# Kernel optimization log

Measured on AMD Instinct MI355X. Metric: run time of the kernel, lower is better.

The kernel has to match this reference:

```python
import jax, jax.numpy as jnp
import numpy as np

N_PTS = 65536   # input points
M = 4096        # sampled clusters (n_nodes)
K = 16          # knn neighbors
C_IN = 128
C_OUT = 256
BN_EPS = 1e-5


def setup_inputs() -> dict:
    key = jax.random.key(0)
    k1, k2, k3 = jax.random.split(key, 3)
    x = jax.random.normal(k1, (N_PTS, C_IN), jnp.float32)
    pos = jax.random.normal(k2, (N_PTS, 3), jnp.float32)
    batch = jnp.zeros((N_PTS,), jnp.int32)  # single point cloud
    W = jax.random.normal(k3, (C_IN, C_OUT), jnp.float32) / np.sqrt(C_IN)
    b = jnp.zeros((C_OUT,), jnp.float32)
    gamma = jnp.ones((C_OUT,), jnp.float32)
    beta = jnp.zeros((C_OUT,), jnp.float32)
    return {"x": x, "pos": pos, "batch": batch, "W": W, "b": b,
            "gamma": gamma, "beta": beta}


def _fps(pos, m):
    """Farthest point sampling starting from index 0. Returns m indices."""
    n = pos.shape[0]

    def step(carry, _):
        min_d, last = carry
        d = jnp.sum((pos - pos[last]) ** 2, axis=-1)  # [N]
        min_d = jnp.minimum(min_d, d)
        nxt = jnp.argmax(min_d).astype(jnp.int32)
        return (min_d, nxt), nxt

    init = (jnp.full((n,), jnp.inf, pos.dtype), jnp.int32(0))
    _, rest = jax.lax.scan(step, init, None, length=m - 1)
    return jnp.concatenate([jnp.zeros((1,), jnp.int32), rest])


def _knn(pos, sub_pos, k):
    """For each of M query points, indices of k nearest points in pos. [M, k]"""
    # squared euclidean distances, [M, N]
    d2 = (jnp.sum(sub_pos ** 2, -1, keepdims=True)
          - 2.0 * sub_pos @ pos.T
          + jnp.sum(pos ** 2, -1)[None, :])
    _, idx = jax.lax.top_k(-d2, k)
    return idx


def _mlp(x, W, b, gamma, beta):
    # Linear -> BatchNorm1d (training-mode batch stats, biased var) -> ReLU
    h = x @ W + b                      # [N, C_OUT]
    mu = jnp.mean(h, axis=0)
    var = jnp.mean((h - mu) ** 2, axis=0)
    h = gamma * (h - mu) * jax.lax.rsqrt(var + BN_EPS) + beta
    return jax.nn.relu(h)


def reference(x, pos, batch, W, b, gamma, beta):
    id_clusters = _fps(pos, M)                 # [M]
    sub_pos = pos[id_clusters]                 # [M, 3]
    sub_batch = batch[id_clusters]             # [M]
    nbr = _knn(pos, sub_pos, K)                # [M, K]
    h = _mlp(x, W, b, gamma, beta)             # [N, C_OUT]
    # gather + max-pool over each cluster's k neighbors (== scatter_max,
    # since knn emits exactly K neighbors per cluster, grouped by cluster)
    out = jnp.max(h[nbr], axis=1)              # [M, C_OUT]
    return out, sub_pos, sub_batch
```

## Files before the change

### kernel.cpp

```cpp
#include <hip/hip_runtime.h>
#include <hip/hip_bf16.h>

#define N_PTS 65536
#define MCLUS 4096
#define KNN   16
#define C_IN  128
#define C_OUT 256

typedef unsigned long long u64;
typedef unsigned u32;

#define WS_ID     0
#define WS_SLOTS  16384
#define WS_BBOX   49152
#define WS_CNT    49216
#define WS_OFS    51264
#define WS_NBR    53312
#define WS_PSUM   315456
#define WS_POS4   315456
#define WS_PSUMSQ 839744
#define WS_SCALE  1364032
#define WS_SHIFT  1365056

__device__ __forceinline__ u32 fkey(float v) {
    u32 u = __float_as_uint(v);
    return (u >> 31) ? ~u : (u | 0x80000000u);
}
__device__ __forceinline__ float funkey(u32 k) {
    u32 u = (k >> 31) ? (k & 0x7FFFFFFFu) : ~k;
    return __uint_as_float(u);
}

__global__ void init_kernel(int* __restrict__ id, u64* __restrict__ slots,
                            u32* __restrict__ bbox, int* __restrict__ cellcnt) {
    int t = threadIdx.x;
    for (int i = t; i < 4096; i += 1024) slots[i] = 0ull;
    if (t < 512) cellcnt[t] = 0;
    if (t < 3)   bbox[t] = 0xFFFFFFFFu;
    if (t >= 3 && t < 6) bbox[t] = 0u;
    if (t == 0) id[0] = 0;
}

__global__ __launch_bounds__(256) void bbox_kernel(const float* __restrict__ pos,
                                                   u32* __restrict__ bbox) {
    int t = blockIdx.x * 256 + threadIdx.x;
    u32 mn0 = 0xFFFFFFFFu, mn1 = 0xFFFFFFFFu, mn2 = 0xFFFFFFFFu;
    u32 mx0 = 0u, mx1 = 0u, mx2 = 0u;
    for (int i = t; i < N_PTS; i += 16384) {
        u32 k0 = fkey(pos[i*3+0]), k1 = fkey(pos[i*3+1]), k2 = fkey(pos[i*3+2]);
        mn0 = min(mn0, k0); mn1 = min(mn1, k1); mn2 = min(mn2, k2);
        mx0 = max(mx0, k0); mx1 = max(mx1, k1); mx2 = max(mx2, k2);
    }
    #pragma unroll
    for (int off = 32; off > 0; off >>= 1) {
        mn0 = min(mn0, (u32)__shfl_xor(mn0, off)); mx0 = max(mx0, (u32)__shfl_xor(mx0, off));
        mn1 = min(mn1, (u32)__shfl_xor(mn1, off)); mx1 = max(mx1, (u32)__shfl_xor(mx1, off));
        mn2 = min(mn2, (u32)__shfl_xor(mn2, off)); mx2 = max(mx2, (u32)__shfl_xor(mx2, off));
    }
    if ((threadIdx.x & 63) == 0) {
        atomicMin(&bbox[0], mn0); atomicMin(&bbox[1], mn1); atomicMin(&bbox[2], mn2);
        atomicMax(&bbox[3], mx0); atomicMax(&bbox[4], mx1); atomicMax(&bbox[5], mx2);
    }
}

__device__ __forceinline__ int cell_of(float x, float y, float z, const u32* bb) {
    float x0 = funkey(bb[0]), y0 = funkey(bb[1]), z0 = funkey(bb[2]);
    float x1 = funkey(bb[3]), y1 = funkey(bb[4]), z1 = funkey(bb[5]);
    float sx = 8.0f / fmaxf(x1 - x0, 1e-20f);
    float sy = 8.0f / fmaxf(y1 - y0, 1e-20f);
    float sz = 8.0f / fmaxf(z1 - z0, 1e-20f);
    int gx = min(max((int)((x - x0) * sx), 0), 7);
    int gy = min(max((int)((y - y0) * sy), 0), 7);
    int gz = min(max((int)((z - z0) * sz), 0), 7);
    int m = 0;
    #pragma unroll
    for (int k = 0; k < 3; ++k)
        m |= (((gx >> k) & 1) << (3*k + 2)) | (((gy >> k) & 1) << (3*k + 1)) | (((gz >> k) & 1) << (3*k));
    return m;
}

__global__ __launch_bounds__(256) void count_kernel(const float* __restrict__ pos,
                                                    const u32* __restrict__ bbox,
                                                    int* __restrict__ cellcnt) {
    int i = blockIdx.x * 256 + threadIdx.x;
    atomicAdd(&cellcnt[cell_of(pos[i*3+0], pos[i*3+1], pos[i*3+2], bbox)], 1);
}

__global__ __launch_bounds__(512) void scan_kernel(const int* __restrict__ cellcnt,
                                                   int* __restrict__ cellofs) {
    __shared__ int tmp[512];
    int t = threadIdx.x;
    int c = cellcnt[t];
    tmp[t] = c; __syncthreads();
    for (int off = 1; off < 512; off <<= 1) {
        int v = (t >= off) ? tmp[t - off] : 0;
        __syncthreads();
        tmp[t] += v;
        __syncthreads();
    }
    cellofs[t] = tmp[t] - c;
}

__global__ __launch_bounds__(256) void scatter_kernel(const float* __restrict__ pos,
                                                      const u32* __restrict__ bbox,
                                                      int* __restrict__ cellofs,
                                                      float4* __restrict__ pos4) {
    int i = blockIdx.x * 256 + threadIdx.x;
    float x = pos[i*3+0], y = pos[i*3+1], z = pos[i*3+2];
    int o = atomicAdd(&cellofs[cell_of(x, y, z, bbox)], 1);
    pos4[o] = make_float4(x, y, z, __int_as_float(i));
}

__device__ __forceinline__ float dist3(float ax, float ay, float az,
                                       float bx, float by, float bz) {
    float dx = __fsub_rn(ax, bx), dy = __fsub_rn(ay, by), dz = __fsub_rn(az, bz);
    return __fadd_rn(__fadd_rn(__fmul_rn(dx, dx), __fmul_rn(dy, dy)), __fmul_rn(dz, dz));
}

__device__ __forceinline__ u32 wave_max_u32(u32 v) {
    #pragma unroll
    for (int off = 32; off > 0; off >>= 1) {
        u32 o = __shfl_xor(v, off);
        v = o > v ? o : v;
    }
    return v;
}
__device__ __forceinline__ u32 wave_min_u32(u32 v) {
    #pragma unroll
    for (int off = 32; off > 0; off >>= 1) {
        u32 o = __shfl_xor(v, off);
        v = o < v ? o : v;
    }
    return v;
}

__device__ __forceinline__ int wave_argmax48(u64 k48) {
    u32 hi = (u32)(k48 >> 16);
    u32 him = wave_max_u32(hi);
    u64 ball = __ballot(hi == him);
    if (__popcll(ball) > 1) {
        u32 a = (hi == him) ? (u32)(k48 & 0xFFFFull) : 0u;
        u32 am = wave_max_u32(a);
        ball = __ballot((hi == him) && (a == am));
    }
    return __ffsll((long long)ball) - 1;
}

__global__ __launch_bounds__(64) void fps_kernel(const float* __restrict__ pos,
                                                 const float4* __restrict__ pos4,
                                                 int* __restrict__ id,
                                                 u64* __restrict__ slots) {
    const int lane = threadIdx.x;
    const int blk  = blockIdx.x;
    __shared__ float bku[1024];

    float px[16], py[16], pz[16], md[16];
    u32 inv[16];
    const float c0x = pos[0], c0y = pos[1], c0z = pos[2];
    #pragma unroll
    for (int e = 0; e < 16; ++e) {
        int sp = blk * 1024 + (lane >> 3) * 128 + e * 8 + (lane & 7);
        float4 v = pos4[sp];
        px[e] = v.x; py[e] = v.y; pz[e] = v.z;
        inv[e] = 0xFFFFu - (u32)__float_as_int(v.w);
        md[e] = dist3(px[e], py[e], pz[e], c0x, c0y, c0z);
    }

    int r = 0;
    u32 fb_mine = 0xFu;

    auto slow_round = [&](int rr, int s) {
        u64 bk = 0; float bx = 0.f, by = 0.f, bz = 0.f;
        #pragma unroll
        for (int e = 0; e < 16; ++e) {
            u64 k = ((u64)__float_as_uint(md[e]) << 16) | inv[e];
            bool bt = k > bk;
            bk = bt ? k : bk; bx = bt ? px[e] : bx; by = bt ? py[e] : by; bz = bt ? pz[e] : bz;
        }
        int src = wave_argmax48(bk);
        float wx = __shfl(bx, src), wy = __shfl(by, src), wz = __shfl(bz, src);
        u64 kb = __shfl(bk, src);

        const u64 tg = (u64)((rr + 1) & 0xFFFF);
        u64* base = &slots[(u32)(rr & 1) * 2048];
        {
            u64 w0 = (kb << 16) | tg;
            u64 w1 = ((u64)__float_as_uint(wx) << 32) | tg;
            u64 w2 = ((u64)__float_as_uint(wy) << 32) | tg;
            u64 w3 = ((u64)__float_as_uint(wz) << 32) | tg;
            u64 wv = (lane == 0) ? w0 : (lane == 1) ? w1 : (lane == 2) ? w2 : w3;
            if (lane < 4)
                __hip_atomic_store(&base[(u32)blk * 32 + (u32)lane], wv,
                                   __ATOMIC_RELAXED, __HIP_MEMORY_SCOPE_AGENT);
        }
        u64* bp = &base[(u32)lane * 32];
        u64 v0, v1, v2, v3;
        for (;;) {
            v0 = __hip_atomic_load(&bp[0], __ATOMIC_RELAXED, __HIP_MEMORY_SCOPE_AGENT);
            v1 = __hip_atomic_load(&bp[1], __ATOMIC_RELAXED, __HIP_MEMORY_SCOPE_AGENT);
            v2 = __hip_atomic_load(&bp[2], __ATOMIC_RELAXED, __HIP_MEMORY_SCOPE_AGENT);
            v3 = __hip_atomic_load(&bp[3], __ATOMIC_RELAXED, __HIP_MEMORY_SCOPE_AGENT);
            u64 bad = ((v0 ^ tg) | (v1 ^ tg) | (v2 ^ tg) | (v3 ^ tg)) & 0xFFFFull;
            if (bad == 0ull) break;
        }
        u64 k2 = v0 >> 16;
        int s2 = wave_argmax48(k2);
        u64 kw = __shfl(k2, s2);
        float cx = __shfl(__uint_as_float((u32)(v1 >> 32)), s2);
        float cy = __shfl(__uint_as_float((u32)(v2 >> 32)), s2);
        float cz = __shfl(__uint_as_float((u32)(v3 >> 32)), s2);
        if (blk == 0 && lane == 0) id[s] = (int)(0xFFFFu - (u32)(kw & 0xFFFFull));
        #pragma unroll
        for (int e = 0; e < 16; ++e)
            md[e] = fminf(md[e], dist3(px[e], py[e], pz[e], cx, cy, cz));
    };

    u64 wk48[8]; float wxa[8], wya[8], wza[8];

    for (int B = 0; B <= 511; ++B) {
        u64 bk = 0; float bx = 0.f, by = 0.f, bz = 0.f;
        #pragma unroll
        for (int e = 0; e < 16; ++e) {
            u64 k = ((u64)__float_as_uint(md[e]) << 16) | inv[e];
            bool bt = k > bk;
            bk = bt ? k : bk; bx = bt ? px[e] : bx; by = bt ? py[e] : by; bz = bt ? pz[e] : bz;
        }
        u64 ks = bk;
        #pragma unroll
        for (int off = 1; off <= 4; off <<= 1) {
            u64 o = __shfl_xor(ks, off);
            if (o > ks) ks = o;
        }
        {
            u64 ball = __ballot(bk == ks);
            int segbase = (lane >> 3) << 3;
            int ssrc = __ffsll((long long)(ball & (0xFFull << segbase))) - 1;
            bx = __shfl(bx, ssrc); by = __shfl(by, ssrc); bz = __shfl(bz, ssrc);
        }

        const u64 tg = (u64)((r + 1) & 0xFFFF);
        u64* base = &slots[(u32)(r & 1) * 2048];
        {
            int c = lane / 3; if (c > 7) c = 7;
            int p = lane - c * 3;
            int srcl = 8 * c;
            u64 kk  = __shfl(ks, srcl);
            float gx = __shfl(bx, srcl), gy = __shfl(by, srcl), gz = __shfl(bz, srcl);
            u32 hi, mid;
            if (p == 0)      { hi = __float_as_uint(gx); mid = (u32)(kk & 0xFFFFull); }
            else if (p == 1) { hi = __float_as_uint(gy); mid = (u32)(kk >> 32) & 0xFFFFu; }
            else             { hi = __float_as_uint(gz); mid = (u32)(kk >> 16) & 0xFFFFu; }
            u64 wd = ((u64)hi << 32) | ((u64)mid << 16) | tg;
            if (lane == 24) wd = ((u64)(fb_mine & 0xFu) << 16) | tg;
            if (lane < 25)
                __hip_atomic_store(&base[(u32)blk * 32 + (u32)lane], wd,
                                   __ATOMIC_RELAXED, __HIP_MEMORY_SCOPE_AGENT);
        }

        u64 w[25]; u32 valid = 0;
        {
            u64* bp = &base[(u32)lane * 32];
            do {
                #pragma unroll
                for (int i = 0; i < 25; ++i)
                    if (!(valid & (1u << i)))
                        w[i] = __hip_atomic_load(&bp[i], __ATOMIC_RELAXED, __HIP_MEMORY_SCOPE_AGENT);
                #pragma unroll
                for (int i = 0; i < 25; ++i)
                    if ((u32)(w[i] & 0xFFFFull) == (u32)tg) valid |= (1u << i);
            } while (valid != 0x1FFFFFFu);
        }
        ++r;

        u32 jstar = wave_min_u32((u32)(w[24] >> 16) & 0xFu);
        if (jstar < 8u) {
            #pragma unroll
            for (int e = 0; e < 16; ++e) md[e] = bku[e * 64 + lane];
            #pragma unroll
            for (int j = 0; j < 8; ++j) {
                if ((u32)j < jstar) {
                    #pragma unroll
                    for (int e = 0; e < 16; ++e)
                        md[e] = fminf(md[e], dist3(px[e], py[e], pz[e], wxa[j], wya[j], wza[j]));
                }
            }
            int sbase = 8 * (B - 1) + 1;
            for (int sub = (int)jstar; sub < 8; ++sub) { slow_round(r, sbase + sub); ++r; }
            fb_mine = 0xFu;
            --B; continue;
        }
        if (B == 511) break;

        float cpx[8], cpy[8], cpz[8], cmdf[8]; u32 cinv[8];
        #pragma unroll
        for (int c = 0; c < 8; ++c) {
            u64 a = w[3 * c], b = w[3 * c + 1], d = w[3 * c + 2];
            cpx[c] = __uint_as_float((u32)(a >> 32));
            cpy[c] = __uint_as_float((u32)(b >> 32));
            cpz[c] = __uint_as_float((u32)(d >> 32));
            cinv[c] = (u32)(a >> 16) & 0xFFFFu;
            u32 mdb = (((u32)(b >> 16) & 0xFFFFu) << 16) | ((u32)(d >> 16) & 0xFFFFu);
            cmdf[c] = __uint_as_float(mdb);
        }

        float pwx = 0.f, pwy = 0.f, pwz = 0.f;
        #pragma unroll
        for (int j = 0; j < 8; ++j) {
            if (j) {
                #pragma unroll
                for (int c = 0; c < 8; ++c)
                    cmdf[c] = fminf(cmdf[c], dist3(cpx[c], cpy[c], cpz[c], pwx, pwy, pwz));
            }
            u64 bk2 = 0; float b2x = 0.f, b2y = 0.f, b2z = 0.f;
            #pragma unroll
            for (int c = 0; c < 8; ++c) {
                u64 k = ((u64)__float_as_uint(cmdf[c]) << 16) | cinv[c];
                bool bt = k > bk2;
                bk2 = bt ? k : bk2; b2x = bt ? cpx[c] : b2x; b2y = bt ? cpy[c] : b2y; b2z = bt ? cpz[c] : b2z;
            }
            int src = wave_argmax48(bk2);
            u64 kw = __shfl(bk2, src);
            float wx = __shfl(b2x, src), wy = __shfl(b2y, src), wz = __shfl(b2z, src);
            wk48[j] = kw; wxa[j] = wx; wya[j] = wy; wza[j] = wz;
            pwx = wx; pwy = wy; pwz = wz;
            if (blk == 0 && lane == 0) id[8 * B + 1 + j] = (int)(0xFFFFu - (u32)(kw & 0xFFFFull));
        }

        #pragma unroll
        for (int e = 0; e < 16; ++e) bku[e * 64 + lane] = md[e];
        u32 vmask = 0;
        #pragma unroll
        for (int j = 0; j < 8; ++j) {
            #pragma unroll
            for (int e = 0; e < 16; ++e) {
                u64 vk = ((u64)__float_as_uint(md[e]) << 16) | inv[e];
                if (vk > wk48[j]) vmask |= (1u << j);
            }
            #pragma unroll
            for (int e = 0; e < 16; ++e)
                md[e] = fminf(md[e], dist3(px[e], py[e], pz[e], wxa[j], wya[j], wza[j]));
        }
        #pragma unroll
        for (int off = 32; off > 0; off >>= 1) vmask |= (u32)__shfl_xor(vmask, off);
        fb_mine = vmask ? (u32)(__ffs(vmask) - 1) : 0xFu;
    }

    for (int s = 4089; s < 4096; ++s) { slow_round(r, s); ++r; }
}

__global__ void subout_kernel(const float* __restrict__ pos, const int* __restrict__ batch,
                              const int* __restrict__ id, float* __restrict__ sub_pos,
                              int* __restrict__ sub_batch) {
    int m = blockIdx.x * blockDim.x + threadIdx.x;
    if (m >= MCLUS) return;
    int idx = id[m];
    sub_pos[m*3+0] = pos[idx*3+0];
    sub_pos[m*3+1] = pos[idx*3+1];
    sub_pos[m*3+2] = pos[idx*3+2];
    sub_batch[m] = batch[idx];
}

__global__ __launch_bounds__(64) void knn_kernel(const float* __restrict__ pos,
                                                 const int* __restrict__ id,
                                                 int* __restrict__ nbr) {
    const int q = blockIdx.x;
    const int lane = threadIdx.x;
    const int qi = id[q];
    const float qx = pos[qi*3+0], qy = pos[qi*3+1], qz = pos[qi*3+2];
    const float nq = __fadd_rn(__fadd_rn(__fmul_rn(qx,qx), __fmul_rn(qy,qy)), __fmul_rn(qz,qz));

    float dl[KNN]; int il[KNN];
    #pragma unroll
    for (int t = 0; t < KNN; ++t) { dl[t] = __builtin_inff(); il[t] = 0x7FFFFFFF; }

    for (int j = lane; j < N_PTS; j += 64) {
        float px = pos[j*3+0], py = pos[j*3+1], pz = pos[j*3+2];
        float npj = __fadd_rn(__fadd_rn(__fmul_rn(px,px), __fmul_rn(py,py)), __fmul_rn(pz,pz));
        float dot = __fadd_rn(__fadd_rn(__fmul_rn(qx,px), __fmul_rn(qy,py)), __fmul_rn(qz,pz));
        float d2  = __fadd_rn(__fsub_rn(nq, __fmul_rn(2.0f, dot)), npj);
        if (d2 < dl[KNN-1] || (d2 == dl[KNN-1] && j < il[KNN-1])) {
            dl[KNN-1] = d2; il[KNN-1] = j;
            #pragma unroll
            for (int t = KNN-1; t > 0; --t) {
                float a = dl[t-1], bq = dl[t];
                int   ai = il[t-1], bi = il[t];
                bool sw = (bq < a) || (bq == a && bi < ai);
                dl[t-1] = sw ? bq : a;  dl[t] = sw ? a : bq;
                il[t-1] = sw ? bi : ai; il[t] = sw ? ai : bi;
            }
        }
    }

    __shared__ float sd[64][KNN];
    __shared__ int   si[64][KNN];
    #pragma unroll
    for (int t = 0; t < KNN; ++t) { sd[lane][t] = dl[t]; si[lane][t] = il[t]; }
    __syncthreads();

    int ptr = 0;
    for (int rr = 0; rr < KNN; ++rr) {
        unsigned long long key = ~0ull;
        if (ptr < KNN) {
            unsigned u = __float_as_uint(sd[lane][ptr]);
            unsigned mu = (u >> 31) ? ~u : (u | 0x80000000u);
            key = ((unsigned long long)mu << 32) | (unsigned)si[lane][ptr];
        }
        unsigned long long m = key;
        #pragma unroll
        for (int off = 32; off > 0; off >>= 1) {
            unsigned long long o = __shfl_xor(m, off);
            if (o < m) m = o;
        }
        if (key == m) ptr++;
        if (lane == 0) nbr[q*KNN + rr] = (int)(m & 0xFFFFFFFFull);
    }
}

__global__ __launch_bounds__(256) void stats_kernel(const float* __restrict__ x,
                                                    const float* __restrict__ W,
                                                    const float* __restrict__ b,
                                                    float* __restrict__ psum,
                                                    float* __restrict__ psumsq) {
    __shared__ float xl[64*128];
    const int tid = threadIdx.x;
    const int cg = (tid & 63) * 4;
    const int rq = tid >> 6;
    float s0=0,s1=0,s2v=0,s3=0, q0=0,q1=0,q2=0,q3=0;
    const float4 bv = *(const float4*)&b[cg];

    for (int t = 0; t < 2; ++t) {
        const size_t row0 = (size_t)blockIdx.x*128 + (size_t)t*64;
        __syncthreads();
        for (int i = tid*4; i < 64*128; i += 1024)
            *(float4*)&xl[i] = *(const float4*)&x[row0*128 + i];
        __syncthreads();

        float acc[16][4];
        #pragma unroll
        for (int rr = 0; rr < 16; ++rr) { acc[rr][0]=bv.x; acc[rr][1]=bv.y; acc[rr][2]=bv.z; acc[rr][3]=bv.w; }

        for (int k4 = 0; k4 < 32; ++k4) {
            float4 w0 = *(const float4*)&W[(k4*4+0)*256 + cg];
            float4 w1 = *(const float4*)&W[(k4*4+1)*256 + cg];
            float4 w2 = *(const float4*)&W[(k4*4+2)*256 + cg];
            float4 w3 = *(const float4*)&W[(k4*4+3)*256 + cg];
            #pragma unroll
            for (int rr = 0; rr < 16; ++rr) {
                float4 xv = *(float4*)&xl[(rq*16+rr)*128 + k4*4];
                acc[rr][0] = fmaf(xv.w,w3.x, fmaf(xv.z,w2.x, fmaf(xv.y,w1.x, fmaf(xv.x,w0.x, acc[rr][0]))));
                acc[rr][1] = fmaf(xv.w,w3.y, fmaf(xv.z,w2.y, fmaf(xv.y,w1.y, fmaf(xv.x,w0.y, acc[rr][1]))));
                acc[rr][2] = fmaf(xv.w,w3.z, fmaf(xv.z,w2.z, fmaf(xv.y,w1.z, fmaf(xv.x,w0.z, acc[rr][2]))));
                acc[rr][3] = fmaf(xv.w,w3.w, fmaf(xv.z,w2.w, fmaf(xv.y,w1.w, fmaf(xv.x,w0.w, acc[rr][3]))));
            }
        }
        #pragma unroll
        for (int rr = 0; rr < 16; ++rr) {
            s0 += acc[rr][0]; q0 = fmaf(acc[rr][0],acc[rr][0],q0);
            s1 += acc[rr][1]; q1 = fmaf(acc[rr][1],acc[rr][1],q1);
            s2v+= acc[rr][2]; q2 = fmaf(acc[rr][2],acc[rr][2],q2);
            s3 += acc[rr][3]; q3 = fmaf(acc[rr][3],acc[rr][3],q3);
        }
    }
    __syncthreads();
    float* red = xl;
    red[rq*256 + cg+0] = s0; red[rq*256 + cg+1] = s1; red[rq*256 + cg+2] = s2v; red[rq*256 + cg+3] = s3;
    red[1024 + rq*256 + cg+0] = q0; red[1024 + rq*256 + cg+1] = q1;
    red[1024 + rq*256 + cg+2] = q2; red[1024 + rq*256 + cg+3] = q3;
    __syncthreads();
    if (rq == 0) {
        #pragma unroll
        for (int c = 0; c < 4; ++c) {
            int ch = cg + c;
            float ss = red[ch] + red[256+ch] + red[512+ch] + red[768+ch];
            float qq = red[1024+ch] + red[1280+ch] + red[1536+ch] + red[1792+ch];
            psum  [blockIdx.x*256 + ch] = ss;
            psumsq[blockIdx.x*256 + ch] = qq;
        }
    }
}

__global__ void finalize_kernel(const float* __restrict__ psum, const float* __restrict__ psumsq,
                                const float* __restrict__ gamma, const float* __restrict__ beta,
                                float* __restrict__ scale, float* __restrict__ shift) {
    int c = threadIdx.x;
    float s = 0.f, s2 = 0.f;
    for (int bl = 0; bl < 512; ++bl) { s += psum[bl*256+c]; s2 += psumsq[bl*256+c]; }
    float mu  = s  / 65536.0f;
    float var = s2 / 65536.0f - mu*mu;
    float inv = rsqrtf(var + 1e-5f);
    float sc = gamma[c] * inv;
    scale[c] = sc;
    shift[c] = beta[c] - mu * sc;
}

__global__ __launch_bounds__(256) void out_kernel(const float* __restrict__ x,
                                                  const float* __restrict__ W,
                                                  const float* __restrict__ b,
                                                  const int* __restrict__ nbr,
                                                  const float* __restrict__ scale,
                                                  const float* __restrict__ shift,
                                                  float* __restrict__ out) {
    __shared__ float xl[16*128];
    __shared__ int nb[16];
    const int tid = threadIdx.x;
    const int m = blockIdx.x;
    if (tid < 16) nb[tid] = nbr[m*16 + tid];
    __syncthreads();
    for (int i = tid; i < 16*128; i += 256) {
        int rr = i >> 7, k = i & 127;
        xl[i] = x[(size_t)nb[rr]*128 + k];
    }
    __syncthreads();

    float acc[16];
    const float bias = b[tid];
    #pragma unroll
    for (int rr = 0; rr < 16; ++rr) acc[rr] = bias;

    for (int k4 = 0; k4 < 32; ++k4) {
        float w0 = W[(k4*4+0)*256 + tid];
        float w1 = W[(k4*4+1)*256 + tid];
        float w2 = W[(k4*4+2)*256 + tid];
        float w3 = W[(k4*4+3)*256 + tid];
        #pragma unroll
        for (int rr = 0; rr < 16; ++rr) {
            float4 xv = *(float4*)&xl[rr*128 + k4*4];
            acc[rr] = fmaf(xv.w,w3, fmaf(xv.z,w2, fmaf(xv.y,w1, fmaf(xv.x,w0, acc[rr]))));
        }
    }
    const float sc = scale[tid], sh = shift[tid];
    float v = acc[0];
    #pragma unroll
    for (int rr = 1; rr < 16; ++rr) v = (sc >= 0.f) ? fmaxf(v, acc[rr]) : fminf(v, acc[rr]);
    out[(size_t)m*256 + tid] = fmaxf(fmaf(sc, v, sh), 0.f);
}

extern "C" void kernel_launch(void* const* d_in, const int* in_sizes, int n_in,
                              void* d_out, int out_size, void* d_ws, size_t ws_size,
                              hipStream_t stream) {
    const float* x     = (const float*)d_in[0];
    const float* pos   = (const float*)d_in[1];
    const int*   batch = (const int*)  d_in[2];
    const float* W     = (const float*)d_in[3];
    const float* b     = (const float*)d_in[4];
    const float* gamma = (const float*)d_in[5];
    const float* beta  = (const float*)d_in[6];

    float* out      = (float*)d_out;
    float* sub_pos  = out + (size_t)MCLUS*C_OUT;
    int*   sub_batch= (int*)(out + (size_t)MCLUS*C_OUT + (size_t)MCLUS*3);

    char* ws = (char*)d_ws;
    int*    id      = (int*)   (ws + WS_ID);
    u64*    slots   = (u64*)   (ws + WS_SLOTS);
    u32*    bbox    = (u32*)   (ws + WS_BBOX);
    int*    cellcnt = (int*)   (ws + WS_CNT);
    int*    cellofs = (int*)   (ws + WS_OFS);
    int*    nbr     = (int*)   (ws + WS_NBR);
    float4* pos4    = (float4*)(ws + WS_POS4);
    float*  psum    = (float*) (ws + WS_PSUM);
    float*  psumsq  = (float*) (ws + WS_PSUMSQ);
    float*  scalep  = (float*) (ws + WS_SCALE);
    float*  shiftp  = (float*) (ws + WS_SHIFT);

    init_kernel<<<1, 1024, 0, stream>>>(id, slots, bbox, cellcnt);
    bbox_kernel<<<64, 256, 0, stream>>>(pos, bbox);
    count_kernel<<<256, 256, 0, stream>>>(pos, bbox, cellcnt);
    scan_kernel<<<1, 512, 0, stream>>>(cellcnt, cellofs);
    scatter_kernel<<<256, 256, 0, stream>>>(pos, bbox, cellofs, pos4);
    fps_kernel<<<64, 64, 0, stream>>>(pos, pos4, id, slots);
    subout_kernel<<<16, 256, 0, stream>>>(pos, batch, id, sub_pos, sub_batch);
    knn_kernel<<<MCLUS, 64, 0, stream>>>(pos, id, nbr);
    stats_kernel<<<512, 256, 0, stream>>>(x, W, b, psum, psumsq);
    finalize_kernel<<<1, 256, 0, stream>>>(psum, psumsq, gamma, beta, scalep, shiftp);
    out_kernel<<<MCLUS, 256, 0, stream>>>(x, W, b, nbr, scalep, shiftp, out);
}
```

Before: 7.865 ms.

## Publish top-2 candidates per segment and resume speculative FPS at first conflict

Each wave segment now publishes its top-2 farthest candidates, giving 16 candidates per block instead of 8, so the speculative batch of 8 FPS picks is more likely to match the true sequence. On a misprediction, the separate slow single-step rounds are replaced by a restart of the speculative batch from the first confirmed mismatch; the tail rounds are folded into the same loop. The slot buffer doubles and the workspace offsets shift to make room. In exchange each exchange round moves more data and polls 49 slots per block instead of 25, and the in-wave selection does more shuffles.

```diff
diff --git a/kernel.cpp b/kernel.cpp
--- a/kernel.cpp
+++ b/kernel.cpp
@@ -12,15 +12,15 @@
 
 #define WS_ID     0
 #define WS_SLOTS  16384
-#define WS_BBOX   49152
-#define WS_CNT    49216
-#define WS_OFS    51264
-#define WS_NBR    53312
-#define WS_PSUM   315456
-#define WS_POS4   315456
-#define WS_PSUMSQ 839744
-#define WS_SCALE  1364032
-#define WS_SHIFT  1365056
+#define WS_BBOX   81920
+#define WS_CNT    81984
+#define WS_OFS    84032
+#define WS_NBR    86080
+#define WS_PSUM   348224
+#define WS_POS4   348224
+#define WS_PSUMSQ 872512
+#define WS_SCALE  1396800
+#define WS_SHIFT  1397824
 
 __device__ __forceinline__ u32 fkey(float v) {
     u32 u = __float_as_uint(v);
@@ -34,7 +34,7 @@
 __global__ void init_kernel(int* __restrict__ id, u64* __restrict__ slots,
                             u32* __restrict__ bbox, int* __restrict__ cellcnt) {
     int t = threadIdx.x;
-    for (int i = t; i < 4096; i += 1024) slots[i] = 0ull;
+    for (int i = t; i < 8192; i += 1024) slots[i] = 0ull;
     if (t < 512) cellcnt[t] = 0;
     if (t < 3)   bbox[t] = 0xFFFFFFFFu;
     if (t >= 3 && t < 6) bbox[t] = 0u;
@@ -168,184 +168,163 @@
 
     int r = 0;
     u32 fb_mine = 0xFu;
-
-    auto slow_round = [&](int rr, int s) {
-        u64 bk = 0; float bx = 0.f, by = 0.f, bz = 0.f;
+    int s_conf = 1;
+    int nsub = 0;
+    u64 wk48[8]; float wxa[8], wya[8], wza[8];
+
+    for (;;) {
+        u64 k1 = 0, k2 = 0;
+        float x1 = px[0], y1 = py[0], z1 = pz[0], x2 = px[0], y2 = py[0], z2 = pz[0];
         #pragma unroll
         for (int e = 0; e < 16; ++e) {
             u64 k = ((u64)__float_as_uint(md[e]) << 16) | inv[e];
-            bool bt = k > bk;
-            bk = bt ? k : bk; bx = bt ? px[e] : bx; by = bt ? py[e] : by; bz = bt ? pz[e] : bz;
-        }
-        int src = wave_argmax48(bk);
-        float wx = __shfl(bx, src), wy = __shfl(by, src), wz = __shfl(bz, src);
-        u64 kb = __shfl(bk, src);
-
-        const u64 tg = (u64)((rr + 1) & 0xFFFF);
-        u64* base = &slots[(u32)(rr & 1) * 2048];
+            bool g1 = k > k1, g2 = k > k2;
+            u64 nk2 = g1 ? k1 : (g2 ? k : k2);
+            float nx2 = g1 ? x1 : (g2 ? px[e] : x2);
+            float ny2 = g1 ? y1 : (g2 ? py[e] : y2);
+            float nz2 = g1 ? z1 : (g2 ? pz[e] : z2);
+            k2 = nk2; x2 = nx2; y2 = ny2; z2 = nz2;
+            k1 = g1 ? k : k1; x1 = g1 ? px[e] : x1; y1 = g1 ? py[e] : y1; z1 = g1 ? pz[e] : z1;
+        }
+        #pragma unroll
+        for (int off = 1; off <= 4; off <<= 1) {
+            u64 ok1 = __shfl_xor(k1, off), ok2 = __shfl_xor(k2, off);
+            float ox1 = __shfl_xor(x1, off), oy1 = __shfl_xor(y1, off), oz1 = __shfl_xor(z1, off);
+            float ox2 = __shfl_xor(x2, off), oy2 = __shfl_xor(y2, off), oz2 = __shfl_xor(z2, off);
+            bool t1 = k1 >= ok1;
+            u64 n1 = t1 ? k1 : ok1; float nx1 = t1 ? x1 : ox1, ny1 = t1 ? y1 : oy1, nz1 = t1 ? z1 : oz1;
+            u64 lo = t1 ? ok1 : k1; float lx = t1 ? ox1 : x1, ly = t1 ? oy1 : y1, lz = t1 ? oz1 : z1;
+            bool t2 = k2 >= ok2;
+            u64 h2 = t2 ? k2 : ok2; float hx = t2 ? x2 : ox2, hy = t2 ? y2 : oy2, hz = t2 ? z2 : oz2;
+            bool t3 = lo >= h2;
+            u64 n2 = t3 ? lo : h2; float nx2 = t3 ? lx : hx, ny2 = t3 ? ly : hy, nz2 = t3 ? lz : hz;
+            k1 = n1; x1 = nx1; y1 = ny1; z1 = nz1;
+            k2 = n2; x2 = nx2; y2 = ny2; z2 = nz2;
+        }
+
+        const u64 tg = (u64)((r + 1) & 0xFFFF);
+        u64* base = &slots[(u32)(r & 1) * 4096];
         {
-            u64 w0 = (kb << 16) | tg;
-            u64 w1 = ((u64)__float_as_uint(wx) << 32) | tg;
-            u64 w2 = ((u64)__float_as_uint(wy) << 32) | tg;
-            u64 w3 = ((u64)__float_as_uint(wz) << 32) | tg;
-            u64 wv = (lane == 0) ? w0 : (lane == 1) ? w1 : (lane == 2) ? w2 : w3;
-            if (lane < 4)
-                __hip_atomic_store(&base[(u32)blk * 32 + (u32)lane], wv,
-                                   __ATOMIC_RELAXED, __HIP_MEMORY_SCOPE_AGENT);
-        }
-        u64* bp = &base[(u32)lane * 32];
-        u64 v0, v1, v2, v3;
-        for (;;) {
-            v0 = __hip_atomic_load(&bp[0], __ATOMIC_RELAXED, __HIP_MEMORY_SCOPE_AGENT);
-            v1 = __hip_atomic_load(&bp[1], __ATOMIC_RELAXED, __HIP_MEMORY_SCOPE_AGENT);
-            v2 = __hip_atomic_load(&bp[2], __ATOMIC_RELAXED, __HIP_MEMORY_SCOPE_AGENT);
-            v3 = __hip_atomic_load(&bp[3], __ATOMIC_RELAXED, __HIP_MEMORY_SCOPE_AGENT);
-            u64 bad = ((v0 ^ tg) | (v1 ^ tg) | (v2 ^ tg) | (v3 ^ tg)) & 0xFFFFull;
-            if (bad == 0ull) break;
-        }
-        u64 k2 = v0 >> 16;
-        int s2 = wave_argmax48(k2);
-        u64 kw = __shfl(k2, s2);
-        float cx = __shfl(__uint_as_float((u32)(v1 >> 32)), s2);
-        float cy = __shfl(__uint_as_float((u32)(v2 >> 32)), s2);
-        float cz = __shfl(__uint_as_float((u32)(v3 >> 32)), s2);
-        if (blk == 0 && lane == 0) id[s] = (int)(0xFFFFu - (u32)(kw & 0xFFFFull));
-        #pragma unroll
-        for (int e = 0; e < 16; ++e)
-            md[e] = fminf(md[e], dist3(px[e], py[e], pz[e], cx, cy, cz));
-    };
-
-    u64 wk48[8]; float wxa[8], wya[8], wza[8];
-
-    for (int B = 0; B <= 511; ++B) {
-        u64 bk = 0; float bx = 0.f, by = 0.f, bz = 0.f;
-        #pragma unroll
-        for (int e = 0; e < 16; ++e) {
-            u64 k = ((u64)__float_as_uint(md[e]) << 16) | inv[e];
-            bool bt = k > bk;
-            bk = bt ? k : bk; bx = bt ? px[e] : bx; by = bt ? py[e] : by; bz = bt ? pz[e] : bz;
-        }
-        u64 ks = bk;
-        #pragma unroll
-        for (int off = 1; off <= 4; off <<= 1) {
-            u64 o = __shfl_xor(ks, off);
-            if (o > ks) ks = o;
-        }
-        {
-            u64 ball = __ballot(bk == ks);
-            int segbase = (lane >> 3) << 3;
-            int ssrc = __ffsll((long long)(ball & (0xFFull << segbase))) - 1;
-            bx = __shfl(bx, ssrc); by = __shfl(by, ssrc); bz = __shfl(bz, ssrc);
-        }
-
-        const u64 tg = (u64)((r + 1) & 0xFFFF);
-        u64* base = &slots[(u32)(r & 1) * 2048];
-        {
-            int c = lane / 3; if (c > 7) c = 7;
+            int c = lane / 3; if (c > 15) c = 15;
             int p = lane - c * 3;
-            int srcl = 8 * c;
-            u64 kk  = __shfl(ks, srcl);
-            float gx = __shfl(bx, srcl), gy = __shfl(by, srcl), gz = __shfl(bz, srcl);
+            int srcl = (c >> 1) * 8;
+            u64 ka = __shfl(k1, srcl), kb = __shfl(k2, srcl);
+            float xa = __shfl(x1, srcl), xb = __shfl(x2, srcl);
+            float ya = __shfl(y1, srcl), yb = __shfl(y2, srcl);
+            float za = __shfl(z1, srcl), zb = __shfl(z2, srcl);
+            u64 kk = (c & 1) ? kb : ka;
+            float gx = (c & 1) ? xb : xa, gy = (c & 1) ? yb : ya, gz = (c & 1) ? zb : za;
             u32 hi, mid;
             if (p == 0)      { hi = __float_as_uint(gx); mid = (u32)(kk & 0xFFFFull); }
             else if (p == 1) { hi = __float_as_uint(gy); mid = (u32)(kk >> 32) & 0xFFFFu; }
             else             { hi = __float_as_uint(gz); mid = (u32)(kk >> 16) & 0xFFFFu; }
             u64 wd = ((u64)hi << 32) | ((u64)mid << 16) | tg;
-            if (lane == 24) wd = ((u64)(fb_mine & 0xFu) << 16) | tg;
-            if (lane < 25)
-                __hip_atomic_store(&base[(u32)blk * 32 + (u32)lane], wd,
+            if (lane == 48) wd = ((u64)(fb_mine & 0xFu) << 16) | tg;
+            if (lane < 49)
+                __hip_atomic_store(&base[(u32)blk * 64 + (u32)lane], wd,
                                    __ATOMIC_RELAXED, __HIP_MEMORY_SCOPE_AGENT);
         }
 
-        u64 w[25]; u32 valid = 0;
+        float cpx[16], cpy[16], cpz[16];
+        u32 cmdb[16], cinv[16], cfb = 0xFu;
+        #pragma unroll
+        for (int c = 0; c < 16; ++c) cmdb[c] = 0u;
         {
-            u64* bp = &base[(u32)lane * 32];
-            do {
+            u64* bp = &base[(u32)lane * 64];
+            u64 valid = 0;
+            const u64 ALL = (1ull << 49) - 1;
+            while (valid != ALL) {
                 #pragma unroll
-                for (int i = 0; i < 25; ++i)
-                    if (!(valid & (1u << i)))
-                        w[i] = __hip_atomic_load(&bp[i], __ATOMIC_RELAXED, __HIP_MEMORY_SCOPE_AGENT);
-                #pragma unroll
-                for (int i = 0; i < 25; ++i)
-                    if ((u32)(w[i] & 0xFFFFull) == (u32)tg) valid |= (1u << i);
-            } while (valid != 0x1FFFFFFu);
+                for (int i = 0; i < 49; ++i) {
+                    if (!((valid >> i) & 1ull)) {
+                        u64 v = __hip_atomic_load(&bp[i], __ATOMIC_RELAXED, __HIP_MEMORY_SCOPE_AGENT);
+                        if ((u32)(v & 0xFFFFull) == (u32)tg) {
+                            valid |= (1ull << i);
+                            u32 hi = (u32)(v >> 32), mid = (u32)(v >> 16) & 0xFFFFu;
+                            if (i == 48) cfb = mid & 0xFu;
+                            else {
+                                const int c = i / 3, p = i - c * 3;
+                                if (p == 0)      { cpx[c] = __uint_as_float(hi); cinv[c] = mid; }
+                                else if (p == 1) { cpy[c] = __uint_as_float(hi); cmdb[c] |= (mid << 16); }
+                                else             { cpz[c] = __uint_as_float(hi); cmdb[c] |= mid; }
+                            }
+                        }
+                    }
+                }
+            }
         }
         ++r;
 
-        u32 jstar = wave_min_u32((u32)(w[24] >> 16) & 0xFu);
-        if (jstar < 8u) {
+        int jg = (int)wave_min_u32(cfb);
+        int js = jg < nsub ? jg : nsub;
+        if (js < nsub) {
             #pragma unroll
             for (int e = 0; e < 16; ++e) md[e] = bku[e * 64 + lane];
             #pragma unroll
             for (int j = 0; j < 8; ++j) {
-                if ((u32)j < jstar) {
+                if (j < js) {
                     #pragma unroll
                     for (int e = 0; e < 16; ++e)
                         md[e] = fminf(md[e], dist3(px[e], py[e], pz[e], wxa[j], wya[j], wza[j]));
                 }
             }
-            int sbase = 8 * (B - 1) + 1;
-            for (int sub = (int)jstar; sub < 8; ++sub) { slow_round(r, sbase + sub); ++r; }
-            fb_mine = 0xFu;
-            --B; continue;
-        }
-        if (B == 511) break;
-
-        float cpx[8], cpy[8], cpz[8], cmdf[8]; u32 cinv[8];
-        #pragma unroll
-        for (int c = 0; c < 8; ++c) {
-            u64 a = w[3 * c], b = w[3 * c + 1], d = w[3 * c + 2];
-            cpx[c] = __uint_as_float((u32)(a >> 32));
-            cpy[c] = __uint_as_float((u32)(b >> 32));
-            cpz[c] = __uint_as_float((u32)(d >> 32));
-            cinv[c] = (u32)(a >> 16) & 0xFFFFu;
-            u32 mdb = (((u32)(b >> 16) & 0xFFFFu) << 16) | ((u32)(d >> 16) & 0xFFFFu);
-            cmdf[c] = __uint_as_float(mdb);
-        }
+            s_conf += js; nsub = 0; fb_mine = 0xFu;
+            continue;
+        }
+        s_conf += nsub;
+        nsub = 0; fb_mine = 0xFu;
+        if (s_conf >= 4096) break;
+        nsub = (4096 - s_conf) < 8 ? (4096 - s_conf) : 8;
+
+        float cmdf[16];
+        #pragma unroll
+        for (int c = 0; c < 16; ++c) cmdf[c] = __uint_as_float(cmdb[c]);
+        #pragma unroll
+        for (int e = 0; e < 16; ++e) bku[e * 64 + lane] = md[e];
 
         float pwx = 0.f, pwy = 0.f, pwz = 0.f;
         #pragma unroll
         for (int j = 0; j < 8; ++j) {
-            if (j) {
+            if (j < nsub) {
+                if (j) {
+                    #pragma unroll
+                    for (int c = 0; c < 16; ++c)
+                        cmdf[c] = fminf(cmdf[c], dist3(cpx[c], cpy[c], cpz[c], pwx, pwy, pwz));
+                }
+                u64 bk2 = 0; float b2x = 0.f, b2y = 0.f, b2z = 0.f;
                 #pragma unroll
-                for (int c = 0; c < 8; ++c)
-                    cmdf[c] = fminf(cmdf[c], dist3(cpx[c], cpy[c], cpz[c], pwx, pwy, pwz));
+                for (int c = 0; c < 16; ++c) {
+                    u64 k = ((u64)__float_as_uint(cmdf[c]) << 16) | cinv[c];
+                    bool bt = k > bk2;
+                    bk2 = bt ? k : bk2; b2x = bt ? cpx[c] : b2x; b2y = bt ? cpy[c] : b2y; b2z = bt ? cpz[c] : b2z;
+                }
+                int src = wave_argmax48(bk2);
+                u64 kw = __shfl(bk2, src);
+                float wx = __shfl(b2x, src), wy = __shfl(b2y, src), wz = __shfl(b2z, src);
+                wk48[j] = kw; wxa[j] = wx; wya[j] = wy; wza[j] = wz;
+                pwx = wx; pwy = wy; pwz = wz;
+                if (blk == 0 && lane == 0) id[s_conf + j] = (int)(0xFFFFu - (u32)(kw & 0xFFFFull));
             }
-            u64 bk2 = 0; float b2x = 0.f, b2y = 0.f, b2z = 0.f;
-            #pragma unroll
-            for (int c = 0; c < 8; ++c) {
-                u64 k = ((u64)__float_as_uint(cmdf[c]) << 16) | cinv[c];
-                bool bt = k > bk2;
-                bk2 = bt ? k : bk2; b2x = bt ? cpx[c] : b2x; b2y = bt ? cpy[c] : b2y; b2z = bt ? cpz[c] : b2z;
+        }
+
+        u32 vmask = 0;
+        #pragma unroll
+        for (int j = 0; j < 8; ++j) {
+            if (j < nsub) {
+                #pragma unroll
+                for (int e = 0; e < 16; ++e) {
+                    u64 vk = ((u64)__float_as_uint(md[e]) << 16) | inv[e];
+                    if (vk > wk48[j]) vmask |= (1u << j);
+                }
+                #pragma unroll
+                for (int e = 0; e < 16; ++e)
+                    md[e] = fminf(md[e], dist3(px[e], py[e], pz[e], wxa[j], wya[j], wza[j]));
             }
-            int src = wave_argmax48(bk2);
-            u64 kw = __shfl(bk2, src);
-            float wx = __shfl(b2x, src), wy = __shfl(b2y, src), wz = __shfl(b2z, src);
-            wk48[j] = kw; wxa[j] = wx; wya[j] = wy; wza[j] = wz;
-            pwx = wx; pwy = wy; pwz = wz;
-            if (blk == 0 && lane == 0) id[8 * B + 1 + j] = (int)(0xFFFFu - (u32)(kw & 0xFFFFull));
-        }
-
-        #pragma unroll
-        for (int e = 0; e < 16; ++e) bku[e * 64 + lane] = md[e];
-        u32 vmask = 0;
-        #pragma unroll
-        for (int j = 0; j < 8; ++j) {
-            #pragma unroll
-            for (int e = 0; e < 16; ++e) {
-                u64 vk = ((u64)__float_as_uint(md[e]) << 16) | inv[e];
-                if (vk > wk48[j]) vmask |= (1u << j);
-            }
-            #pragma unroll
-            for (int e = 0; e < 16; ++e)
-                md[e] = fminf(md[e], dist3(px[e], py[e], pz[e], wxa[j], wya[j], wza[j]));
         }
         #pragma unroll
         for (int off = 32; off > 0; off >>= 1) vmask |= (u32)__shfl_xor(vmask, off);
         fb_mine = vmask ? (u32)(__ffs(vmask) - 1) : 0xFu;
     }
-
-    for (int s = 4089; s < 4096; ++s) { slow_round(r, s); ++r; }
 }
 
 __global__ void subout_kernel(const float* __restrict__ pos, const int* __restrict__ batch,
```

New measurement: 12.94 ms. +64.5%, slower.
